# Performance work log

Hardware: AMD Instinct MI355X
Metric: run time of the kernel (lower is better)

The kernel has to match this reference:

```python
import jax, jax.numpy as jnp
import numpy as np

P = 7            # pooling_size
SCALE = 1.0 / 16  # spatial_scale


def _roi_align(feat, tf):
    # feat: [B,C,T,H,W] (L2-normalized), tf: [N,7] = [b, x1, y1, t1, x2, y2, t2]
    # RoIAlignAvg with temporal pooled size == T (identity in time): bilinear
    # sample at each spatial bin center for every frame.
    H, W = feat.shape[-2], feat.shape[-1]
    b = tf[:, 0].astype(jnp.int32)
    x1, y1 = tf[:, 1] * SCALE, tf[:, 2] * SCALE
    x2, y2 = tf[:, 4] * SCALE, tf[:, 5] * SCALE
    bw = jnp.maximum(x2 - x1 + SCALE, 1e-3) / P
    bh = jnp.maximum(y2 - y1 + SCALE, 1e-3) / P
    ctr = jnp.arange(P, dtype=feat.dtype) + 0.5
    xs = jnp.clip(x1[:, None] + ctr * bw[:, None], 0.0, W - 1)  # [N,P]
    ys = jnp.clip(y1[:, None] + ctr * bh[:, None], 0.0, H - 1)  # [N,P]
    x0 = jnp.floor(xs); y0 = jnp.floor(ys)
    fx = xs - x0; fy = ys - y0
    x0i = x0.astype(jnp.int32); x1i = jnp.minimum(x0i + 1, W - 1)
    y0i = y0.astype(jnp.int32); y1i = jnp.minimum(y0i + 1, H - 1)

    def g(yi, xi):
        # advanced indices broadcast to [N,P,P]; result [N,P,P,C,T]
        return feat[b[:, None, None], :, :, yi[:, :, None], xi[:, None, :]]

    wy0 = (1 - fy)[:, :, None, None, None]; wy1 = fy[:, :, None, None, None]
    wx0 = (1 - fx)[:, None, :, None, None]; wx1 = fx[:, None, :, None, None]
    out = (wy0 * wx0 * g(y0i, x0i) + wy0 * wx1 * g(y0i, x1i)
           + wy1 * wx0 * g(y1i, x0i) + wy1 * wx1 * g(y1i, x1i))
    return jnp.transpose(out, (0, 3, 4, 1, 2))  # [N,C,T,P,P]


def _forward(base_feat, tubes, gt_rois, gt_tubes, conv_w, conv_b, w1, b1, w2, b2, wp, bp):
    B, C, T = base_feat.shape[:3]
    R = tubes.shape[1]
    # F.normalize(base_feat, p=2, dim=1)
    feat = base_feat / jnp.maximum(
        jnp.linalg.norm(base_feat, axis=1, keepdims=True), 1e-12)

    # --- ragged scatter: rois[b,i,t1:t2+1,1:] = tubes[b,i,[1,2,4,5]] ---
    f = jnp.arange(T)
    f_off = (f[None, :] + jnp.arange(B)[:, None] * T).astype(tubes.dtype)  # [B,T]
    t1 = tubes[..., 3].astype(jnp.int32)[..., None]
    t2 = tubes[..., 6].astype(jnp.int32)[..., None]
    mask = (f[None, None, :] >= t1) & (f[None, None, :] <= t2)  # [B,R,T]
    box = tubes[..., jnp.array([1, 2, 4, 5])]                   # [B,R,4]
    rois_box = jnp.where(mask[..., None], box[:, :, None, :],
                         jnp.zeros((), tubes.dtype))
    rois = jnp.concatenate(
        [jnp.broadcast_to(f_off[:, None, :, None], (B, R, T, 1)), rois_box], -1)

    # --- RoIAlign + AvgPool3d over T + head (eval mode: dropout = identity) ---
    pooled = _roi_align(feat, tubes.reshape(-1, 7))  # [N,C,T,P,P]
    pooled = pooled.mean(axis=2)                     # [N,C,P,P]
    x = jnp.einsum('nchw,oc->nohw', pooled, conv_w) + conv_b[None, :, None, None]
    x = x.reshape(x.shape[0], -1)                    # [N, C*P*P]
    x = jax.nn.relu(x @ w1 + b1)
    x = jax.nn.relu(x @ w2 + b2)
    bbox_pred = x @ wp + bp                          # [N, 4*T]
    return bbox_pred, pooled, rois


def setup_inputs() -> dict:
    B, R, T, C, HF, IMG = 4, 64, 16, 256, 14, 224
    ks = jax.random.split(jax.random.key(0), 16)
    base_feat = jax.random.normal(ks[0], (B, C, T, HF, HF), jnp.float32)
    x1 = jax.random.uniform(ks[1], (B, R), minval=0.0, maxval=IMG / 2)
    y1 = jax.random.uniform(ks[2], (B, R), minval=0.0, maxval=IMG / 2)
    x2 = jnp.minimum(x1 + jax.random.uniform(ks[3], (B, R), minval=16.0, maxval=IMG / 2), IMG - 1.0)
    y2 = jnp.minimum(y1 + jax.random.uniform(ks[4], (B, R), minval=16.0, maxval=IMG / 2), IMG - 1.0)
    tt = jax.random.randint(ks[5], (B, R, 2), 0, T)
    t1 = jnp.min(tt, -1).astype(jnp.float32)
    t2 = jnp.max(tt, -1).astype(jnp.float32)
    bidx = jnp.broadcast_to(jnp.arange(B)[:, None], (B, R)).astype(jnp.float32)
    tubes = jnp.stack([bidx, x1, y1, t1, x2, y2, t2], -1)
    s = 0.02
    return {
        'base_feat': base_feat,
        'tubes': tubes,
        'gt_rois': jax.random.normal(ks[6], (B, 10, T, 5), jnp.float32),
        'gt_tubes': jax.random.normal(ks[7], (B, 10, 7), jnp.float32),
        'conv_w': jax.random.normal(ks[8], (C, C), jnp.float32) * s,
        'conv_b': jnp.zeros((C,), jnp.float32),
        'w1': jax.random.normal(ks[9], (C * P * P, 2048), jnp.float32) * s,
        'b1': jnp.zeros((2048,), jnp.float32),
        'w2': jax.random.normal(ks[10], (2048, 512), jnp.float32) * s,
        'b2': jnp.zeros((512,), jnp.float32),
        'wp': jax.random.normal(ks[11], (512, 4 * T), jnp.float32) * s,
        'bp': jnp.zeros((4 * T,), jnp.float32),
    }


def reference(base_feat, tubes, gt_rois, gt_tubes, conv_w, conv_b, w1, b1, w2, b2, wp, bp):
    return _forward(base_feat, tubes, gt_rois, gt_tubes, conv_w, conv_b, w1, b1, w2, b2, wp, bp)
```

## Files before the change

### kernel.cpp

```cpp
#include <hip/hip_runtime.h>

#define HH 14
#define WW 14
#define HWSZ 196
#define TT 16
#define CC 256
#define BB 4
#define RR 64
#define NROI 256
#define PP 7
#define PP2 49

typedef short s4v __attribute__((ext_vector_type(4)));
typedef short s8v __attribute__((ext_vector_type(8)));
typedef float f4v __attribute__((ext_vector_type(4)));

__device__ inline ushort f2bf(float f) {
    union { float f; unsigned u; } v; v.f = f;
    unsigned r = v.u + 0x7fffu + ((v.u >> 16) & 1u);
    return (ushort)(r >> 16);
}

__global__ void k_sumsq(const float* __restrict__ base, float* __restrict__ partial) {
    int blk = blockIdx.x;
    int bt = blk >> 3, cg = blk & 7;
    int hw = threadIdx.x;
    if (hw >= HWSZ) return;
    int b = bt >> 4, t = bt & 15;
    const float* p = base + ((size_t)(b * CC + cg * 32) * TT + t) * HWSZ + hw;
    float s = 0.f;
    #pragma unroll 8
    for (int c = 0; c < 32; ++c) {
        float v = p[(size_t)c * TT * HWSZ];
        s += v * v;
    }
    partial[cg * 12544 + bt * HWSZ + hw] = s;
}

__global__ void k_finish_inv(const float* __restrict__ partial, float* __restrict__ inv) {
    int j = blockIdx.x * 256 + threadIdx.x;
    if (j >= 12544) return;
    float s = 0.f;
    #pragma unroll
    for (int cg = 0; cg < 8; ++cg) s += partial[cg * 12544 + j];
    inv[j] = 1.0f / fmaxf(sqrtf(s), 1e-12f);
}

__global__ void k_tsum(const float* __restrict__ base, const float* __restrict__ inv,
                       float* __restrict__ tsum) {
    int bc = blockIdx.x;
    int hw = threadIdx.x;
    if (hw >= HWSZ) return;
    int b = bc >> 8;
    const float* p = base + (size_t)bc * TT * HWSZ + hw;
    const float* iv = inv + b * TT * HWSZ + hw;
    float s = 0.f;
    #pragma unroll
    for (int t = 0; t < TT; ++t) s += p[t * HWSZ] * iv[t * HWSZ];
    tsum[(size_t)bc * HWSZ + hw] = s;
}

__global__ void k_roialign(const float* __restrict__ tubes, const float* __restrict__ tsum,
                           float* __restrict__ pooled, float* __restrict__ pooledT,
                           float* __restrict__ rois) {
    __shared__ int sx0[PP], sx1[PP], sy0[PP], sy1[PP];
    __shared__ float sfx[PP], sfy[PP];
    __shared__ int sb;
    int n = blockIdx.x;
    int tid = threadIdx.x;
    if (tid < PP) {
        const float* tb = tubes + n * 7;
        float x1 = tb[1] * 0.0625f, y1 = tb[2] * 0.0625f;
        float x2 = tb[4] * 0.0625f, y2 = tb[5] * 0.0625f;
        float bw = fmaxf(x2 - x1 + 0.0625f, 0.001f) * (1.0f / PP);
        float bh = fmaxf(y2 - y1 + 0.0625f, 0.001f) * (1.0f / PP);
        float ctr = tid + 0.5f;
        float xs = fminf(fmaxf(x1 + ctr * bw, 0.f), (float)(WW - 1));
        float ys = fminf(fmaxf(y1 + ctr * bh, 0.f), (float)(HH - 1));
        float x0f = floorf(xs), y0f = floorf(ys);
        int x0 = (int)x0f, y0 = (int)y0f;
        sx0[tid] = x0; sx1[tid] = min(x0 + 1, WW - 1);
        sy0[tid] = y0; sy1[tid] = min(y0 + 1, HH - 1);
        sfx[tid] = xs - x0f; sfy[tid] = ys - y0f;
        if (tid == 0) sb = (int)tb[0];
    }
    if (tid < TT) {
        const float* tb = tubes + n * 7;
        int t1 = (int)tb[3], t2 = (int)tb[6];
        bool m = (tid >= t1) && (tid <= t2);
        int b = n >> 6;
        float* o = rois + ((size_t)n * TT + tid) * 5;
        o[0] = (float)(b * TT + tid);
        o[1] = m ? tb[1] : 0.f;
        o[2] = m ? tb[2] : 0.f;
        o[3] = m ? tb[4] : 0.f;
        o[4] = m ? tb[5] : 0.f;
    }
    __syncthreads();
    const float* tbase = tsum + (size_t)sb * CC * HWSZ;

    for (int idx = tid; idx < CC * PP2; idx += 256) {
        int c = idx / PP2, bin = idx - (idx / PP2) * PP2;
        int py = bin / PP, px = bin - (bin / PP) * PP;
        const float* tp = tbase + (size_t)c * HWSZ;
        float fx = sfx[px], fy = sfy[py];
        int y0 = sy0[py] * WW, y1 = sy1[py] * WW;
        float v00 = tp[y0 + sx0[px]];
        float v01 = tp[y0 + sx1[px]];
        float v10 = tp[y1 + sx0[px]];
        float v11 = tp[y1 + sx1[px]];
        float v = (1.f - fy) * ((1.f - fx) * v00 + fx * v01)
                + fy        * ((1.f - fx) * v10 + fx * v11);
        pooled[(size_t)n * CC * PP2 + idx] = v * (1.0f / TT);
    }
    for (int idx = tid; idx < PP2 * CC; idx += 256) {
        int bin = idx >> 8, c = idx & 255;
        int py = bin / PP, px = bin - (bin / PP) * PP;
        const float* tp = tbase + (size_t)c * HWSZ;
        float fx = sfx[px], fy = sfy[py];
        int y0 = sy0[py] * WW, y1 = sy1[py] * WW;
        float v00 = tp[y0 + sx0[px]];
        float v01 = tp[y0 + sx1[px]];
        float v10 = tp[y1 + sx0[px]];
        float v11 = tp[y1 + sx1[px]];
        float v = (1.f - fy) * ((1.f - fx) * v00 + fx * v01)
                + fy        * ((1.f - fx) * v10 + fx * v11);
        pooledT[((size_t)n * PP2 + bin) * CC + c] = v * (1.0f / TT);
    }
}

__global__ __launch_bounds__(256) void gemm64(const float* __restrict__ A,
                                              const float* __restrict__ B_,
                                              float* __restrict__ Cp,
                                              int M, int N, int K,
                                              int lda, int ldb, int kChunk) {
    __shared__ float As[16][64];
    __shared__ float Bs[16][68];
    int m0 = blockIdx.x * 64, n0 = blockIdx.y * 64;
    int s = blockIdx.z;
    int k0 = s * kChunk, kend = k0 + kChunk;
    int tid = threadIdx.x;
    int am = tid >> 2, ak = (tid & 3) << 2;
    int bk = tid >> 4, bn = (tid & 15) << 2;
    int tm = tid >> 4, tn = tid & 15;
    float acc[4][4] = {};
    const float* Aptr = A + (size_t)(m0 + am) * lda + ak;
    const float* Bptr = B_ + (size_t)bk * ldb + n0 + bn;

    for (int kk = k0; kk < kend; kk += 16) {
        float4 av = *(const float4*)(Aptr + kk);
        float4 bv = *(const float4*)(Bptr + (size_t)kk * ldb);
        __syncthreads();
        As[ak + 0][am] = av.x;
        As[ak + 1][am] = av.y;
        As[ak + 2][am] = av.z;
        As[ak + 3][am] = av.w;
        *(float4*)&Bs[bk][bn] = bv;
        __syncthreads();
        #pragma unroll
        for (int k = 0; k < 16; ++k) {
            float4 a = *(const float4*)&As[k][tm << 2];
            float4 b = *(const float4*)&Bs[k][tn << 2];
            float a4[4] = {a.x, a.y, a.z, a.w};
            float b4[4] = {b.x, b.y, b.z, b.w};
            #pragma unroll
            for (int i = 0; i < 4; ++i)
                #pragma unroll
                for (int j = 0; j < 4; ++j)
                    acc[i][j] += a4[i] * b4[j];
        }
    }
    float* Cs = Cp + (size_t)s * M * N;
    #pragma unroll
    for (int i = 0; i < 4; ++i) {
        float4 v = make_float4(acc[i][0], acc[i][1], acc[i][2], acc[i][3]);
        *(float4*)&Cs[(size_t)(m0 + (tm << 2) + i) * N + n0 + (tn << 2)] = v;
    }
}

__global__ void k_reduce(const float* __restrict__ part, const float* __restrict__ bias,
                         float* __restrict__ out, int MN, int N, int S, int relu) {
    int idx = blockIdx.x * 256 + threadIdx.x;
    if (idx >= MN) return;
    float s = bias[idx % N];
    for (int i = 0; i < S; ++i) s += part[(size_t)i * MN + idx];
    if (relu) s = fmaxf(s, 0.f);
    out[idx] = s;
}

__global__ __launch_bounds__(512) void conv_mfma(const float* __restrict__ pooledT,
                                                 const float* __restrict__ conv_w,
                                                 const float* __restrict__ conv_b,
                                                 ushort* __restrict__ xb) {
    __shared__ __align__(16) ushort Ab[2][8192];
    __shared__ __align__(16) ushort Bres[8192];
    const int m0 = blockIdx.x * 256, o0 = blockIdx.y * 64;
    const int tid = threadIdx.x;
    const int lane = tid & 63, w = tid >> 6;
    const int wm = w & 3, wn = w >> 2;
    const int fr = lane & 15, fg = lane >> 4;

    for (int ii = tid; ii < 2048; ii += 512) {
        int o_l = ii >> 5, cq = ii & 31;
        const float* s = conv_w + (size_t)(o0 + o_l) * 256 + cq * 8;
        float4 v0 = *(const float4*)s;
        float4 v1 = *(const float4*)(s + 4);
        float vv[8] = {v0.x, v0.y, v0.z, v0.w, v1.x, v1.y, v1.z, v1.w};
        int dbase = (cq >> 2) * 2048 + (o_l >> 4) * 512 + (cq & 3) * 128 + (o_l & 15);
        #pragma unroll
        for (int jc = 0; jc < 8; ++jc) Bres[dbase + jc * 16] = f2bf(vv[jc]);
    }

    int ii0 = tid, ii1 = 512 + tid, ii2 = 1024 + tid, ii3 = 1536 + tid;
    const float* pA0 = pooledT + (size_t)(m0 + (ii0 >> 3)) * 256 + (ii0 & 7) * 4;
    const float* pA1 = pooledT + (size_t)(m0 + (ii1 >> 3)) * 256 + (ii1 & 7) * 4;
    const float* pA2 = pooledT + (size_t)(m0 + (ii2 >> 3)) * 256 + (ii2 & 7) * 4;
    const float* pA3 = pooledT + (size_t)(m0 + (ii3 >> 3)) * 256 + (ii3 & 7) * 4;
#define CDOFF(ii) (((ii >> 3) >> 4) * 512 + ((ii & 7) >> 1) * 128 + ((ii >> 3) & 15) * 8 + (ii & 1) * 4)
    const int do0 = CDOFF(ii0), do1 = CDOFF(ii1), do2 = CDOFF(ii2), do3 = CDOFF(ii3);
#undef CDOFF
    float4 a0_, a1_, a2_, a3_;
#define CONV_LOAD(t) do { a0_ = *(const float4*)(pA0 + (t) * 32); \
                          a1_ = *(const float4*)(pA1 + (t) * 32); \
                          a2_ = *(const float4*)(pA2 + (t) * 32); \
                          a3_ = *(const float4*)(pA3 + (t) * 32); } while (0)
#define W4(dst, v) do { s4v _u; _u[0]=(short)f2bf((v).x); _u[1]=(short)f2bf((v).y); \
                        _u[2]=(short)f2bf((v).z); _u[3]=(short)f2bf((v).w); \
                        *(s4v*)(dst) = _u; } while (0)
#define CONV_WRITE(buf) do { W4(Ab[buf] + do0, a0_); W4(Ab[buf] + do1, a1_); \
                             W4(Ab[buf] + do2, a2_); W4(Ab[buf] + do3, a3_); } while (0)

    CONV_LOAD(0);
    CONV_WRITE(0);
    __syncthreads();

    const int aoff = wm * 2048 + fg * 128 + fr * 8;
    f4v acc[4][2];
    #pragma unroll
    for (int i = 0; i < 4; ++i)
        #pragma unroll
        for (int j = 0; j < 2; ++j) acc[i][j] = (f4v){0.f, 0.f, 0.f, 0.f};

    for (int t = 0; t < 8; ++t) {
        if (t < 7) CONV_LOAD(t + 1);
        const ushort* A = Ab[t & 1];
        s8v a0 = *(const s8v*)(A + aoff);
        s8v a1 = *(const s8v*)(A + aoff + 512);
        s8v a2 = *(const s8v*)(A + aoff + 1024);
        s8v a3 = *(const s8v*)(A + aoff + 1536);
        unsigned bbase = (unsigned)(size_t)(&Bres[0]) + t * 4096 + wn * 2048 + fg * 256 + fr * 2;
        s4v bl0, bh0, bl1, bh1;
        asm volatile("ds_read_b64_tr_b16 %0, %2\n\t"
                     "ds_read_b64_tr_b16 %1, %2 offset:128"
                     : "=v"(bl0), "=v"(bh0) : "v"(bbase));
        asm volatile("ds_read_b64_tr_b16 %0, %2 offset:1024\n\t"
                     "ds_read_b64_tr_b16 %1, %2 offset:1152"
                     : "=v"(bl1), "=v"(bh1) : "v"(bbase));
        asm volatile("s_waitcnt lgkmcnt(0)" ::: "memory");
        __builtin_amdgcn_sched_barrier(0);
        s8v b0, b1;
        b0[0] = bl0[0]; b0[1] = bl0[1]; b0[2] = bl0[2]; b0[3] = bl0[3];
        b0[4] = bh0[0]; b0[5] = bh0[1]; b0[6] = bh0[2]; b0[7] = bh0[3];
        b1[0] = bl1[0]; b1[1] = bl1[1]; b1[2] = bl1[2]; b1[3] = bl1[3];
        b1[4] = bh1[0]; b1[5] = bh1[1]; b1[6] = bh1[2]; b1[7] = bh1[3];
        acc[0][0] = __builtin_amdgcn_mfma_f32_16x16x32_bf16(a0, b0, acc[0][0], 0, 0, 0);
        acc[0][1] = __builtin_amdgcn_mfma_f32_16x16x32_bf16(a0, b1, acc[0][1], 0, 0, 0);
        acc[1][0] = __builtin_amdgcn_mfma_f32_16x16x32_bf16(a1, b0, acc[1][0], 0, 0, 0);
        acc[1][1] = __builtin_amdgcn_mfma_f32_16x16x32_bf16(a1, b1, acc[1][1], 0, 0, 0);
        acc[2][0] = __builtin_amdgcn_mfma_f32_16x16x32_bf16(a2, b0, acc[2][0], 0, 0, 0);
        acc[2][1] = __builtin_amdgcn_mfma_f32_16x16x32_bf16(a2, b1, acc[2][1], 0, 0, 0);
        acc[3][0] = __builtin_amdgcn_mfma_f32_16x16x32_bf16(a3, b0, acc[3][0], 0, 0, 0);
        acc[3][1] = __builtin_amdgcn_mfma_f32_16x16x32_bf16(a3, b1, acc[3][1], 0, 0, 0);
        if (t < 7) CONV_WRITE((t + 1) & 1);
        __syncthreads();
    }
#undef CONV_LOAD
#undef CONV_WRITE
#undef W4

    #pragma unroll
    for (int ni = 0; ni < 2; ++ni) {
        int o = o0 + wn * 32 + ni * 16 + fr;
        float cb = conv_b[o];
        int obase = (o >> 5) * 8192 + (((o >> 3) & 3)) * 128 + (o & 7);
        #pragma unroll
        for (int mi = 0; mi < 4; ++mi)
            #pragma unroll
            for (int i = 0; i < 4; ++i) {
                int gm = m0 + wm * 64 + mi * 16 + fg * 4 + i;
                int n = gm / 49, hw = gm - n * 49;
                xb[(size_t)hw * 65536 + obase + (n >> 4) * 512 + (n & 15) * 8]
                    = f2bf(acc[mi][ni][i] + cb);
            }
    }
}

__global__ __launch_bounds__(512) void fc1_mfma(const ushort* __restrict__ xb,
                                                const float* __restrict__ w1,
                                                float* __restrict__ part) {
    __shared__ __align__(16) ushort Ab[4][8192];
    __shared__ __align__(16) ushort Bbf[2][2048];
    const int s = blockIdx.x, nblk = blockIdx.y;
    const int n0 = nblk * 64;
    const int k0 = s * 1568;
    const int tid = threadIdx.x;
    const int lane = tid & 63, w = tid >> 6;
    const int wm = w & 3, wn = w >> 2;
    const int fr = lane & 15, fg = lane >> 4;

    const ushort* gA = xb + (size_t)s * 49 * 8192;
    const int slot0 = tid, slot1 = 512 + tid;

    const int kr = (w >> 2) * 16 + (lane >> 2);
    const int bnb = w & 3, bnq = lane & 3;
    const int ncol = n0 + bnb * 16 + bnq * 4;
    const int bw_u = bnb * 512 + kr * 16 + bnq * 4;

    const int aoff = wm * 2048 + fg * 128 + fr * 8;
    f4v acc[4][2];
    #pragma unroll
    for (int i = 0; i < 4; ++i)
        #pragma unroll
        for (int j = 0; j < 2; ++j) acc[i][j] = (f4v){0.f, 0.f, 0.f, 0.f};

#define STAGE_A(buf, kg) do {                                                                   \
    ushort* _d = Ab[buf];                                                                       \
    __builtin_amdgcn_global_load_lds(                                                           \
        (const __attribute__((address_space(1))) void*)(gA + (size_t)(kg) * 8192 + slot0 * 8),  \
        (__attribute__((address_space(3))) void*)(_d + slot0 * 8), 16, 0, 0);                   \
    __builtin_amdgcn_global_load_lds(                                                           \
        (const __attribute__((address_space(1))) void*)(gA + (size_t)(kg) * 8192 + slot1 * 8),  \
        (__attribute__((address_space(3))) void*)(_d + slot1 * 8), 16, 0, 0);                   \
} while (0)
#define GBP(t) (*(const float4*)(w1 +                                                           \
    (size_t)(((unsigned)(k0 + (t) * 32 + kr) & 255u) * 49 +                                     \
             ((unsigned)(k0 + (t) * 32 + kr) >> 8)) * 2048 + ncol))
#define BWRITE(buf, rb) do {                                                                    \
    s4v _u; _u[0] = (short)f2bf((rb).x); _u[1] = (short)f2bf((rb).y);                           \
    _u[2] = (short)f2bf((rb).z); _u[3] = (short)f2bf((rb).w);                                   \
    *(s4v*)&Bbf[buf][bw_u] = _u;                                                                \
} while (0)

    float4 rb0, rb1, rb2, rb3;
    STAGE_A(0, 0);
    STAGE_A(1, 1);
    rb0 = GBP(0); rb1 = GBP(1); rb2 = GBP(2); rb3 = GBP(3);
    BWRITE(0, rb0);
    __builtin_amdgcn_sched_barrier(0);
    asm volatile("s_waitcnt vmcnt(3) lgkmcnt(0)" ::: "memory");
    __builtin_amdgcn_s_barrier();
    __builtin_amdgcn_sched_barrier(0);

#define FC1_BODY(t, rbL, rbU) do {                                                              \
    int kg2 = (t) + 2 > 48 ? 48 : (t) + 2;                                                      \
    int kg4 = (t) + 4 > 48 ? 48 : (t) + 4;                                                      \
    STAGE_A(((t) + 2) & 3, kg2);                                                                \
    __builtin_amdgcn_sched_barrier(0);                                                          \
    rbL = GBP(kg4);                                                                             \
    __builtin_amdgcn_sched_barrier(0);                                                          \
    const ushort* _A = Ab[(t) & 3];                                                             \
    s8v _a0 = *(const s8v*)(_A + aoff);                                                         \
    s8v _a1 = *(const s8v*)(_A + aoff + 512);                                                   \
    s8v _a2 = *(const s8v*)(_A + aoff + 1024);                                                  \
    s8v _a3 = *(const s8v*)(_A + aoff + 1536);                                                  \
    unsigned _bb = (unsigned)(size_t)(&Bbf[(t) & 1][0]) + wn * 2048 + fg * 256 + fr * 2;        \
    s4v _bl0, _bh0, _bl1, _bh1;                                                                 \
    asm volatile("ds_read_b64_tr_b16 %0, %2\n\t"                                                \
                 "ds_read_b64_tr_b16 %1, %2 offset:128"                                         \
                 : "=v"(_bl0), "=v"(_bh0) : "v"(_bb));                                          \
    asm volatile("ds_read_b64_tr_b16 %0, %2 offset:1024\n\t"                                    \
                 "ds_read_b64_tr_b16 %1, %2 offset:1152"                                        \
                 : "=v"(_bl1), "=v"(_bh1) : "v"(_bb));                                          \
    asm volatile("s_waitcnt lgkmcnt(0)" ::: "memory");                                          \
    __builtin_amdgcn_sched_barrier(0);                                                          \
    s8v _b0, _b1;                                                                               \
    _b0[0]=_bl0[0]; _b0[1]=_bl0[1]; _b0[2]=_bl0[2]; _b0[3]=_bl0[3];                             \
    _b0[4]=_bh0[0]; _b0[5]=_bh0[1]; _b0[6]=_bh0[2]; _b0[7]=_bh0[3];                             \
    _b1[0]=_bl1[0]; _b1[1]=_bl1[1]; _b1[2]=_bl1[2]; _b1[3]=_bl1[3];                             \
    _b1[4]=_bh1[0]; _b1[5]=_bh1[1]; _b1[6]=_bh1[2]; _b1[7]=_bh1[3];                             \
    acc[0][0] = __builtin_amdgcn_mfma_f32_16x16x32_bf16(_a0, _b0, acc[0][0], 0, 0, 0);          \
    acc[0][1] = __builtin_amdgcn_mfma_f32_16x16x32_bf16(_a0, _b1, acc[0][1], 0, 0, 0);          \
    acc[1][0] = __builtin_amdgcn_mfma_f32_16x16x32_bf16(_a1, _b0, acc[1][0], 0, 0, 0);          \
    acc[1][1] = __builtin_amdgcn_mfma_f32_16x16x32_bf16(_a1, _b1, acc[1][1], 0, 0, 0);          \
    acc[2][0] = __builtin_amdgcn_mfma_f32_16x16x32_bf16(_a2, _b0, acc[2][0], 0, 0, 0);          \
    acc[2][1] = __builtin_amdgcn_mfma_f32_16x16x32_bf16(_a2, _b1, acc[2][1], 0, 0, 0);          \
    acc[3][0] = __builtin_amdgcn_mfma_f32_16x16x32_bf16(_a3, _b0, acc[3][0], 0, 0, 0);          \
    acc[3][1] = __builtin_amdgcn_mfma_f32_16x16x32_bf16(_a3, _b1, acc[3][1], 0, 0, 0);          \
    BWRITE(((t) + 1) & 1, rbU);                                                                 \
    __builtin_amdgcn_sched_barrier(0);                                                          \
    asm volatile("s_waitcnt vmcnt(4) lgkmcnt(0)" ::: "memory");                                 \
    __builtin_amdgcn_s_barrier();                                                               \
    __builtin_amdgcn_sched_barrier(0);                                                          \
} while (0)

    for (int tb = 0; tb < 44; tb += 4) {
        FC1_BODY(tb + 0, rb0, rb1);
        FC1_BODY(tb + 1, rb1, rb2);
        FC1_BODY(tb + 2, rb2, rb3);
        FC1_BODY(tb + 3, rb3, rb0);
    }
    FC1_BODY(44, rb0, rb1);
    FC1_BODY(45, rb1, rb2);
    FC1_BODY(46, rb2, rb3);
    FC1_BODY(47, rb3, rb0);

    {
        const ushort* _A = Ab[0];
        s8v _a0 = *(const s8v*)(_A + aoff);
        s8v _a1 = *(const s8v*)(_A + aoff + 512);
        s8v _a2 = *(const s8v*)(_A + aoff + 1024);
        s8v _a3 = *(const s8v*)(_A + aoff + 1536);
        unsigned _bb = (unsigned)(size_t)(&Bbf[0][0]) + wn * 2048 + fg * 256 + fr * 2;
        s4v _bl0, _bh0, _bl1, _bh1;
        asm volatile("ds_read_b64_tr_b16 %0, %2\n\t"
                     "ds_read_b64_tr_b16 %1, %2 offset:128"
                     : "=v"(_bl0), "=v"(_bh0) : "v"(_bb));
        asm volatile("ds_read_b64_tr_b16 %0, %2 offset:1024\n\t"
                     "ds_read_b64_tr_b16 %1, %2 offset:1152"
                     : "=v"(_bl1), "=v"(_bh1) : "v"(_bb));
        asm volatile("s_waitcnt lgkmcnt(0)" ::: "memory");
        __builtin_amdgcn_sched_barrier(0);
        s8v _b0, _b1;
        _b0[0]=_bl0[0]; _b0[1]=_bl0[1]; _b0[2]=_bl0[2]; _b0[3]=_bl0[3];
        _b0[4]=_bh0[0]; _b0[5]=_bh0[1]; _b0[6]=_bh0[2]; _b0[7]=_bh0[3];
        _b1[0]=_bl1[0]; _b1[1]=_bl1[1]; _b1[2]=_bl1[2]; _b1[3]=_bl1[3];
        _b1[4]=_bh1[0]; _b1[5]=_bh1[1]; _b1[6]=_bh1[2]; _b1[7]=_bh1[3];
        acc[0][0] = __builtin_amdgcn_mfma_f32_16x16x32_bf16(_a0, _b0, acc[0][0], 0, 0, 0);
        acc[0][1] = __builtin_amdgcn_mfma_f32_16x16x32_bf16(_a0, _b1, acc[0][1], 0, 0, 0);
        acc[1][0] = __builtin_amdgcn_mfma_f32_16x16x32_bf16(_a1, _b0, acc[1][0], 0, 0, 0);
        acc[1][1] = __builtin_amdgcn_mfma_f32_16x16x32_bf16(_a1, _b1, acc[1][1], 0, 0, 0);
        acc[2][0] = __builtin_amdgcn_mfma_f32_16x16x32_bf16(_a2, _b0, acc[2][0], 0, 0, 0);
        acc[2][1] = __builtin_amdgcn_mfma_f32_16x16x32_bf16(_a2, _b1, acc[2][1], 0, 0, 0);
        acc[3][0] = __builtin_amdgcn_mfma_f32_16x16x32_bf16(_a3, _b0, acc[3][0], 0, 0, 0);
        acc[3][1] = __builtin_amdgcn_mfma_f32_16x16x32_bf16(_a3, _b1, acc[3][1], 0, 0, 0);
    }
#undef FC1_BODY
#undef STAGE_A
#undef GBP
#undef BWRITE

    float* dst = part + (size_t)s * 256 * 2048 + n0 + wn * 32 + fr;
    #pragma unroll
    for (int mi = 0; mi < 4; ++mi)
        #pragma unroll
        for (int ni = 0; ni < 2; ++ni)
            #pragma unroll
            for (int i = 0; i < 4; ++i) {
                int row = wm * 64 + mi * 16 + fg * 4 + i;
                dst[(size_t)row * 2048 + ni * 16] = acc[mi][ni][i];
            }
}

extern "C" void kernel_launch(void* const* d_in, const int* in_sizes, int n_in,
                              void* d_out, int out_size, void* d_ws, size_t ws_size,
                              hipStream_t stream) {
    const float* base   = (const float*)d_in[0];
    const float* tubes  = (const float*)d_in[1];
    const float* conv_w = (const float*)d_in[4];
    const float* conv_b = (const float*)d_in[5];
    const float* w1     = (const float*)d_in[6];
    const float* b1     = (const float*)d_in[7];
    const float* w2     = (const float*)d_in[8];
    const float* b2     = (const float*)d_in[9];
    const float* wp     = (const float*)d_in[10];
    const float* bp     = (const float*)d_in[11];

    float* out    = (float*)d_out;
    float* bbox   = out;
    float* pooled = out + 16384;
    float* rois   = out + 16384 + 3211264;

    float* ws      = (float*)d_ws;
    float* inv     = ws;
    float* partial = ws + 12544;
    float* tsum    = ws + 112896;
    float* pooledT = ws + 313600;
    ushort* xb     = (ushort*)(ws + 3524864);
    float* h1      = ws + 6736128;
    float* h2      = ws + 7260416;
    float* part    = ws + 7391488;

    k_sumsq<<<BB * TT * 8, 256, 0, stream>>>(base, partial);
    k_finish_inv<<<49, 256, 0, stream>>>(partial, inv);
    k_tsum<<<BB * CC, 256, 0, stream>>>(base, inv, tsum);
    k_roialign<<<NROI, 256, 0, stream>>>(tubes, tsum, pooled, pooledT, rois);

    conv_mfma<<<dim3(49, 4), 512, 0, stream>>>(pooledT, conv_w, conv_b, xb);

    fc1_mfma<<<dim3(8, 32), 512, 0, stream>>>(xb, w1, part);
    k_reduce<<<(256 * 2048 + 255) / 256, 256, 0, stream>>>(part, b1, h1, 256 * 2048, 2048, 8, 1);

    gemm64<<<dim3(4, 8, 8), 256, 0, stream>>>(h1, w2, part,
                                              256, 512, 2048, 2048, 512, 256);
    k_reduce<<<(256 * 512 + 255) / 256, 256, 0, stream>>>(part, b2, h2, 256 * 512, 512, 8, 1);

    gemm64<<<dim3(4, 1, 8), 256, 0, stream>>>(h2, wp, part,
                                              256, 64, 512, 512, 64, 64);
    k_reduce<<<(256 * 64 + 255) / 256, 256, 0, stream>>>(part, bp, bbox, 256 * 64, 64, 8, 0);
}
```

Measured before the change: 125.9 us.

## Load fc1 A operand directly to registers, store bf16 partials, fuse small fc3

The fc1 kernel stops staging the A operand through LDS with global_load_lds and instead loads each wave's A fragments from global memory straight into registers, double-buffered across iterations. Its split-K partial sums are now written as bf16, and a matching reduce kernel reads them, which halves the partial traffic. The final 512x64 layer now runs in one small direct kernel instead of a split-K gemm plus a reduce. The costs are lower precision in the fc1 partial accumulation and a simpler, less tuned synchronisation in the fc1 loop.

Result: slower. 130.1 us (+3.4%).

```diff
diff --git a/kernel.cpp b/kernel.cpp
--- a/kernel.cpp
+++ b/kernel.cpp
@@ -19,6 +19,10 @@
     union { float f; unsigned u; } v; v.f = f;
     unsigned r = v.u + 0x7fffu + ((v.u >> 16) & 1u);
     return (ushort)(r >> 16);
+}
+__device__ inline float bf2f(ushort u) {
+    union { unsigned u; float f; } v; v.u = ((unsigned)u) << 16;
+    return v.f;
 }
 
 __global__ void k_sumsq(const float* __restrict__ base, float* __restrict__ partial) {
@@ -186,6 +190,16 @@
     for (int i = 0; i < S; ++i) s += part[(size_t)i * MN + idx];
     if (relu) s = fmaxf(s, 0.f);
     out[idx] = s;
+}
+
+__global__ void k_reduce_bf(const ushort* __restrict__ part, const float* __restrict__ bias,
+                            float* __restrict__ out) {
+    int idx = blockIdx.x * 256 + threadIdx.x;
+    if (idx >= 256 * 2048) return;
+    float s = bias[idx & 2047];
+    #pragma unroll
+    for (int i = 0; i < 8; ++i) s += bf2f(part[(size_t)i * 524288 + idx]);
+    out[idx] = fmaxf(s, 0.f);
 }
 
 __global__ __launch_bounds__(512) void conv_mfma(const float* __restrict__ pooledT,
@@ -297,8 +311,7 @@
 
 __global__ __launch_bounds__(512) void fc1_mfma(const ushort* __restrict__ xb,
                                                 const float* __restrict__ w1,
-                                                float* __restrict__ part) {
-    __shared__ __align__(16) ushort Ab[4][8192];
+                                                ushort* __restrict__ partb) {
     __shared__ __align__(16) ushort Bbf[2][2048];
     const int s = blockIdx.x, nblk = blockIdx.y;
     const int n0 = nblk * 64;
@@ -309,7 +322,6 @@
     const int fr = lane & 15, fg = lane >> 4;
 
     const ushort* gA = xb + (size_t)s * 49 * 8192;
-    const int slot0 = tid, slot1 = 512 + tid;
 
     const int kr = (w >> 2) * 16 + (lane >> 2);
     const int bnb = w & 3, bnq = lane & 3;
@@ -323,15 +335,6 @@
         #pragma unroll
         for (int j = 0; j < 2; ++j) acc[i][j] = (f4v){0.f, 0.f, 0.f, 0.f};
 
-#define STAGE_A(buf, kg) do {                                                                   \
-    ushort* _d = Ab[buf];                                                                       \
-    __builtin_amdgcn_global_load_lds(                                                           \
-        (const __attribute__((address_space(1))) void*)(gA + (size_t)(kg) * 8192 + slot0 * 8),  \
-        (__attribute__((address_space(3))) void*)(_d + slot0 * 8), 16, 0, 0);                   \
-    __builtin_amdgcn_global_load_lds(                                                           \
-        (const __attribute__((address_space(1))) void*)(gA + (size_t)(kg) * 8192 + slot1 * 8),  \
-        (__attribute__((address_space(3))) void*)(_d + slot1 * 8), 16, 0, 0);                   \
-} while (0)
 #define GBP(t) (*(const float4*)(w1 +                                                           \
     (size_t)(((unsigned)(k0 + (t) * 32 + kr) & 255u) * 49 +                                     \
              ((unsigned)(k0 + (t) * 32 + kr) >> 8)) * 2048 + ncol))
@@ -341,28 +344,29 @@
     *(s4v*)&Bbf[buf][bw_u] = _u;                                                                \
 } while (0)
 
+    s8v aA0, aA1, aA2, aA3, aB0, aB1, aB2, aB3;
     float4 rb0, rb1, rb2, rb3;
-    STAGE_A(0, 0);
-    STAGE_A(1, 1);
+
+    {
+        const ushort* _g0 = gA;
+        aA0 = *(const s8v*)(_g0 + aoff);
+        aA1 = *(const s8v*)(_g0 + aoff + 512);
+        aA2 = *(const s8v*)(_g0 + aoff + 1024);
+        aA3 = *(const s8v*)(_g0 + aoff + 1536);
+    }
     rb0 = GBP(0); rb1 = GBP(1); rb2 = GBP(2); rb3 = GBP(3);
     BWRITE(0, rb0);
-    __builtin_amdgcn_sched_barrier(0);
-    asm volatile("s_waitcnt vmcnt(3) lgkmcnt(0)" ::: "memory");
-    __builtin_amdgcn_s_barrier();
-    __builtin_amdgcn_sched_barrier(0);
-
-#define FC1_BODY(t, rbL, rbU) do {                                                              \
-    int kg2 = (t) + 2 > 48 ? 48 : (t) + 2;                                                      \
+    __syncthreads();
+
+#define FC1_BODY(t, rbL, rbU, aC0, aC1, aC2, aC3, aN0, aN1, aN2, aN3) do {                      \
+    int kg1 = (t) + 1 > 48 ? 48 : (t) + 1;                                                      \
     int kg4 = (t) + 4 > 48 ? 48 : (t) + 4;                                                      \
-    STAGE_A(((t) + 2) & 3, kg2);                                                                \
-    __builtin_amdgcn_sched_barrier(0);                                                          \
+    const ushort* _gn = gA + (size_t)kg1 * 8192;                                                \
+    aN0 = *(const s8v*)(_gn + aoff);                                                            \
+    aN1 = *(const s8v*)(_gn + aoff + 512);                                                      \
+    aN2 = *(const s8v*)(_gn + aoff + 1024);                                                     \
+    aN3 = *(const s8v*)(_gn + aoff + 1536);                                                     \
     rbL = GBP(kg4);                                                                             \
-    __builtin_amdgcn_sched_barrier(0);                                                          \
-    const ushort* _A = Ab[(t) & 3];                                                             \
-    s8v _a0 = *(const s8v*)(_A + aoff);                                                         \
-    s8v _a1 = *(const s8v*)(_A + aoff + 512);                                                   \
-    s8v _a2 = *(const s8v*)(_A + aoff + 1024);                                                  \
-    s8v _a3 = *(const s8v*)(_A + aoff + 1536);                                                  \
     unsigned _bb = (unsigned)(size_t)(&Bbf[(t) & 1][0]) + wn * 2048 + fg * 256 + fr * 2;        \
     s4v _bl0, _bh0, _bl1, _bh1;                                                                 \
     asm volatile("ds_read_b64_tr_b16 %0, %2\n\t"                                                \
@@ -378,38 +382,26 @@
     _b0[4]=_bh0[0]; _b0[5]=_bh0[1]; _b0[6]=_bh0[2]; _b0[7]=_bh0[3];                             \
     _b1[0]=_bl1[0]; _b1[1]=_bl1[1]; _b1[2]=_bl1[2]; _b1[3]=_bl1[3];                             \
     _b1[4]=_bh1[0]; _b1[5]=_bh1[1]; _b1[6]=_bh1[2]; _b1[7]=_bh1[3];                             \
-    acc[0][0] = __builtin_amdgcn_mfma_f32_16x16x32_bf16(_a0, _b0, acc[0][0], 0, 0, 0);          \
-    acc[0][1] = __builtin_amdgcn_mfma_f32_16x16x32_bf16(_a0, _b1, acc[0][1], 0, 0, 0);          \
-    acc[1][0] = __builtin_amdgcn_mfma_f32_16x16x32_bf16(_a1, _b0, acc[1][0], 0, 0, 0);          \
-    acc[1][1] = __builtin_amdgcn_mfma_f32_16x16x32_bf16(_a1, _b1, acc[1][1], 0, 0, 0);          \
-    acc[2][0] = __builtin_amdgcn_mfma_f32_16x16x32_bf16(_a2, _b0, acc[2][0], 0, 0, 0);          \
-    acc[2][1] = __builtin_amdgcn_mfma_f32_16x16x32_bf16(_a2, _b1, acc[2][1], 0, 0, 0);          \
-    acc[3][0] = __builtin_amdgcn_mfma_f32_16x16x32_bf16(_a3, _b0, acc[3][0], 0, 0, 0);          \
-    acc[3][1] = __builtin_amdgcn_mfma_f32_16x16x32_bf16(_a3, _b1, acc[3][1], 0, 0, 0);          \
+    acc[0][0] = __builtin_amdgcn_mfma_f32_16x16x32_bf16(aC0, _b0, acc[0][0], 0, 0, 0);          \
+    acc[0][1] = __builtin_amdgcn_mfma_f32_16x16x32_bf16(aC0, _b1, acc[0][1], 0, 0, 0);          \
+    acc[1][0] = __builtin_amdgcn_mfma_f32_16x16x32_bf16(aC1, _b0, acc[1][0], 0, 0, 0);          \
+    acc[1][1] = __builtin_amdgcn_mfma_f32_16x16x32_bf16(aC1, _b1, acc[1][1], 0, 0, 0);          \
+    acc[2][0] = __builtin_amdgcn_mfma_f32_16x16x32_bf16(aC2, _b0, acc[2][0], 0, 0, 0);          \
+    acc[2][1] = __builtin_amdgcn_mfma_f32_16x16x32_bf16(aC2, _b1, acc[2][1], 0, 0, 0);          \
+    acc[3][0] = __builtin_amdgcn_mfma_f32_16x16x32_bf16(aC3, _b0, acc[3][0], 0, 0, 0);          \
+    acc[3][1] = __builtin_amdgcn_mfma_f32_16x16x32_bf16(aC3, _b1, acc[3][1], 0, 0, 0);          \
     BWRITE(((t) + 1) & 1, rbU);                                                                 \
-    __builtin_amdgcn_sched_barrier(0);                                                          \
-    asm volatile("s_waitcnt vmcnt(4) lgkmcnt(0)" ::: "memory");                                 \
-    __builtin_amdgcn_s_barrier();                                                               \
-    __builtin_amdgcn_sched_barrier(0);                                                          \
+    __syncthreads();                                                                            \
 } while (0)
 
-    for (int tb = 0; tb < 44; tb += 4) {
-        FC1_BODY(tb + 0, rb0, rb1);
-        FC1_BODY(tb + 1, rb1, rb2);
-        FC1_BODY(tb + 2, rb2, rb3);
-        FC1_BODY(tb + 3, rb3, rb0);
-    }
-    FC1_BODY(44, rb0, rb1);
-    FC1_BODY(45, rb1, rb2);
-    FC1_BODY(46, rb2, rb3);
-    FC1_BODY(47, rb3, rb0);
+    for (int tb = 0; tb < 48; tb += 4) {
+        FC1_BODY(tb + 0, rb0, rb1, aA0, aA1, aA2, aA3, aB0, aB1, aB2, aB3);
+        FC1_BODY(tb + 1, rb1, rb2, aB0, aB1, aB2, aB3, aA0, aA1, aA2, aA3);
+        FC1_BODY(tb + 2, rb2, rb3, aA0, aA1, aA2, aA3, aB0, aB1, aB2, aB3);
+        FC1_BODY(tb + 3, rb3, rb0, aB0, aB1, aB2, aB3, aA0, aA1, aA2, aA3);
+    }
 
     {
-        const ushort* _A = Ab[0];
-        s8v _a0 = *(const s8v*)(_A + aoff);
-        s8v _a1 = *(const s8v*)(_A + aoff + 512);
-        s8v _a2 = *(const s8v*)(_A + aoff + 1024);
-        s8v _a3 = *(const s8v*)(_A + aoff + 1536);
         unsigned _bb = (unsigned)(size_t)(&Bbf[0][0]) + wn * 2048 + fg * 256 + fr * 2;
         s4v _bl0, _bh0, _bl1, _bh1;
         asm volatile("ds_read_b64_tr_b16 %0, %2\n\t"
@@ -425,21 +417,20 @@
         _b0[4]=_bh0[0]; _b0[5]=_bh0[1]; _b0[6]=_bh0[2]; _b0[7]=_bh0[3];
         _b1[0]=_bl1[0]; _b1[1]=_bl1[1]; _b1[2]=_bl1[2]; _b1[3]=_bl1[3];
         _b1[4]=_bh1[0]; _b1[5]=_bh1[1]; _b1[6]=_bh1[2]; _b1[7]=_bh1[3];
-        acc[0][0] = __builtin_amdgcn_mfma_f32_16x16x32_bf16(_a0, _b0, acc[0][0], 0, 0, 0);
-        acc[0][1] = __builtin_amdgcn_mfma_f32_16x16x32_bf16(_a0, _b1, acc[0][1], 0, 0, 0);
-        acc[1][0] = __builtin_amdgcn_mfma_f32_16x16x32_bf16(_a1, _b0, acc[1][0], 0, 0, 0);
-        acc[1][1] = __builtin_amdgcn_mfma_f32_16x16x32_bf16(_a1, _b1, acc[1][1], 0, 0, 0);
-        acc[2][0] = __builtin_amdgcn_mfma_f32_16x16x32_bf16(_a2, _b0, acc[2][0], 0, 0, 0);
-        acc[2][1] = __builtin_amdgcn_mfma_f32_16x16x32_bf16(_a2, _b1, acc[2][1], 0, 0, 0);
-        acc[3][0] = __builtin_amdgcn_mfma_f32_16x16x32_bf16(_a3, _b0, acc[3][0], 0, 0, 0);
-        acc[3][1] = __builtin_amdgcn_mfma_f32_16x16x32_bf16(_a3, _b1, acc[3][1], 0, 0, 0);
+        acc[0][0] = __builtin_amdgcn_mfma_f32_16x16x32_bf16(aA0, _b0, acc[0][0], 0, 0, 0);
+        acc[0][1] = __builtin_amdgcn_mfma_f32_16x16x32_bf16(aA0, _b1, acc[0][1], 0, 0, 0);
+        acc[1][0] = __builtin_amdgcn_mfma_f32_16x16x32_bf16(aA1, _b0, acc[1][0], 0, 0, 0);
+        acc[1][1] = __builtin_amdgcn_mfma_f32_16x16x32_bf16(aA1, _b1, acc[1][1], 0, 0, 0);
+        acc[2][0] = __builtin_amdgcn_mfma_f32_16x16x32_bf16(aA2, _b0, acc[2][0], 0, 0, 0);
+        acc[2][1] = __builtin_amdgcn_mfma_f32_16x16x32_bf16(aA2, _b1, acc[2][1], 0, 0, 0);
+        acc[3][0] = __builtin_amdgcn_mfma_f32_16x16x32_bf16(aA3, _b0, acc[3][0], 0, 0, 0);
+        acc[3][1] = __builtin_amdgcn_mfma_f32_16x16x32_bf16(aA3, _b1, acc[3][1], 0, 0, 0);
     }
 #undef FC1_BODY
-#undef STAGE_A
 #undef GBP
 #undef BWRITE
 
-    float* dst = part + (size_t)s * 256 * 2048 + n0 + wn * 32 + fr;
+    ushort* dst = partb + (size_t)s * 524288 + n0 + wn * 32 + fr;
     #pragma unroll
     for (int mi = 0; mi < 4; ++mi)
         #pragma unroll
@@ -447,8 +438,32 @@
             #pragma unroll
             for (int i = 0; i < 4; ++i) {
                 int row = wm * 64 + mi * 16 + fg * 4 + i;
-                dst[(size_t)row * 2048 + ni * 16] = acc[mi][ni][i];
+                dst[(size_t)row * 2048 + ni * 16] = f2bf(acc[mi][ni][i]);
             }
+}
+
+__global__ __launch_bounds__(256) void fc3_small(const float* __restrict__ h2,
+                                                 const float* __restrict__ wp,
+                                                 const float* __restrict__ bp,
+                                                 float* __restrict__ bbox) {
+    __shared__ float sh2[8][512];
+    int blk = blockIdx.x;
+    int tid = threadIdx.x;
+    int n = tid & 63;
+    int mr = tid >> 6;
+    int m0 = blk * 8;
+    for (int i = tid; i < 8 * 512; i += 256)
+        sh2[i >> 9][i & 511] = h2[(size_t)(m0 + (i >> 9)) * 512 + (i & 511)];
+    __syncthreads();
+    float b = bp[n];
+    float acc0 = b, acc1 = b;
+    for (int k = 0; k < 512; ++k) {
+        float wv = wp[k * 64 + n];
+        acc0 += sh2[mr][k] * wv;
+        acc1 += sh2[mr + 4][k] * wv;
+    }
+    bbox[(size_t)(m0 + mr) * 64 + n] = acc0;
+    bbox[(size_t)(m0 + mr + 4) * 64 + n] = acc1;
 }
 
 extern "C" void kernel_launch(void* const* d_in, const int* in_sizes, int n_in,
@@ -479,6 +494,7 @@
     float* h1      = ws + 6736128;
     float* h2      = ws + 7260416;
     float* part    = ws + 7391488;
+    ushort* partb  = (ushort*)part;
 
     k_sumsq<<<BB * TT * 8, 256, 0, stream>>>(base, partial);
     k_finish_inv<<<49, 256, 0, stream>>>(partial, inv);
@@ -487,14 +503,12 @@
 
     conv_mfma<<<dim3(49, 4), 512, 0, stream>>>(pooledT, conv_w, conv_b, xb);
 
-    fc1_mfma<<<dim3(8, 32), 512, 0, stream>>>(xb, w1, part);
-    k_reduce<<<(256 * 2048 + 255) / 256, 256, 0, stream>>>(part, b1, h1, 256 * 2048, 2048, 8, 1);
+    fc1_mfma<<<dim3(8, 32), 512, 0, stream>>>(xb, w1, partb);
+    k_reduce_bf<<<2048, 256, 0, stream>>>(partb, b1, h1);
 
     gemm64<<<dim3(4, 8, 8), 256, 0, stream>>>(h1, w2, part,
                                               256, 512, 2048, 2048, 512, 256);
     k_reduce<<<(256 * 512 + 255) / 256, 256, 0, stream>>>(part, b2, h2, 256 * 512, 512, 8, 1);
 
-    gemm64<<<dim3(4, 1, 8), 256, 0, stream>>>(h2, wp, part,
-                                              256, 64, 512, 512, 64, 64);
-    k_reduce<<<(256 * 64 + 255) / 256, 256, 0, stream>>>(part, bp, bbox, 256 * 64, 64, 8, 0);
-}
+    fc3_small<<<32, 256, 0, stream>>>(h2, wp, bp, bbox);
+}
```
